# Kernel tuning notes

Measured on AMD Instinct MI355X. Metric: run time of the kernel, lower is better.

The kernel has to match this reference:

```python
import jax, jax.numpy as jnp
import numpy as np

LEAKY_SLOPE = 0.01  # torch.nn.LeakyReLU default negative_slope

N_NODES = 100000
LATENT = 64
N_EDGES = 3200000
HIDDEN = 32


def setup_inputs() -> dict:
    key = jax.random.key(0)
    k_z, k_e0, k_e1, k_w1, k_b1, k_w2, k_b2 = jax.random.split(key, 7)
    z = jax.random.normal(k_z, (N_NODES, LATENT), dtype=jnp.float32)
    edge_idx = jnp.stack([
        jax.random.randint(k_e0, (N_EDGES,), 0, N_NODES),
        jax.random.randint(k_e1, (N_EDGES,), 0, N_NODES),
    ]).astype(jnp.int64 if jax.config.jax_enable_x64 else jnp.int32)
    in_dim = 2 * LATENT
    # torch Linear default init: U(-1/sqrt(fan_in), 1/sqrt(fan_in))
    s1 = 1.0 / np.sqrt(in_dim)
    s2 = 1.0 / np.sqrt(HIDDEN)
    W1 = jax.random.uniform(k_w1, (in_dim, HIDDEN), minval=-s1, maxval=s1, dtype=jnp.float32)
    b1 = jax.random.uniform(k_b1, (HIDDEN,), minval=-s1, maxval=s1, dtype=jnp.float32)
    W2 = jax.random.uniform(k_w2, (HIDDEN, 1), minval=-s2, maxval=s2, dtype=jnp.float32)
    b2 = jax.random.uniform(k_b2, (1,), minval=-s2, maxval=s2, dtype=jnp.float32)
    return {"z": z, "edge_idx": edge_idx, "W1": W1, "b1": b1, "W2": W2, "b2": b2}


def reference(z, edge_idx, W1, b1, W2, b2):
    # Gather node pairs and concat: [E, 2*latent_dim]
    node_pairs = jnp.concatenate([z[edge_idx[0]], z[edge_idx[1]]], axis=1)
    # Linear -> LeakyReLU (Dropout is identity at inference) -> Linear -> tanh
    h = node_pairs @ W1 + b1                    # [E, hidden]
    h = jnp.where(h >= 0, h, LEAKY_SLOPE * h)   # LeakyReLU
    out = h @ W2 + b2                           # [E, 1]
    return jnp.tanh(out)
```

## Files before the change

### kernel.cpp

```cpp
#include <hip/hip_runtime.h>
#include <hip/hip_fp16.h>
#include <math.h>

#define LEAKY 0.01f

__device__ inline float fast_tanh(float x) {
    float e2 = __expf(2.0f * x);
    return 1.0f - 2.0f * __builtin_amdgcn_rcpf(e2 + 1.0f);
}

__device__ inline float2 h2f(uint w) {
    __half2 h = *reinterpret_cast<__half2*>(&w);
    return __half22float2(h);
}

__global__ __launch_bounds__(256) void node_proj_g4(
    const float* __restrict__ z, const float* __restrict__ W1,
    const float* __restrict__ b1, __half* __restrict__ U, __half* __restrict__ V,
    int N)
{
    __shared__ float w1s[128 * 32];

    {
        const float4* src = reinterpret_cast<const float4*>(W1);
        float4* dst = reinterpret_cast<float4*>(w1s);
        int tid = threadIdx.x;
        #pragma unroll
        for (int i = 0; i < 4; ++i) dst[tid + 256 * i] = src[tid + 256 * i];
    }
    __syncthreads();

    int t = blockIdx.x * blockDim.x + threadIdx.x;
    int n = t >> 2;
    int g = t & 3;
    if (n >= N) return;

    const float4* zr = reinterpret_cast<const float4*>(z + (size_t)n * 64);

    float au[8], av[8];
    #pragma unroll
    for (int j = 0; j < 8; ++j) { au[j] = b1[g * 8 + j]; av[j] = 0.0f; }

    #pragma unroll 4
    for (int k4 = 0; k4 < 16; ++k4) {
        float4 a = zr[k4];
        #pragma unroll
        for (int c = 0; c < 4; ++c) {
            int k = 4 * k4 + c;
            float zk = (c == 0) ? a.x : (c == 1) ? a.y : (c == 2) ? a.z : a.w;
            const float4* wu = reinterpret_cast<const float4*>(&w1s[k * 32 + g * 8]);
            const float4* wv = reinterpret_cast<const float4*>(&w1s[(64 + k) * 32 + g * 8]);
            float4 wu0 = wu[0], wu1 = wu[1];
            float4 wv0 = wv[0], wv1 = wv[1];
            au[0] = fmaf(zk, wu0.x, au[0]);
            au[1] = fmaf(zk, wu0.y, au[1]);
            au[2] = fmaf(zk, wu0.z, au[2]);
            au[3] = fmaf(zk, wu0.w, au[3]);
            au[4] = fmaf(zk, wu1.x, au[4]);
            au[5] = fmaf(zk, wu1.y, au[5]);
            au[6] = fmaf(zk, wu1.z, au[6]);
            au[7] = fmaf(zk, wu1.w, au[7]);
            av[0] = fmaf(zk, wv0.x, av[0]);
            av[1] = fmaf(zk, wv0.y, av[1]);
            av[2] = fmaf(zk, wv0.z, av[2]);
            av[3] = fmaf(zk, wv0.w, av[3]);
            av[4] = fmaf(zk, wv1.x, av[4]);
            av[5] = fmaf(zk, wv1.y, av[5]);
            av[6] = fmaf(zk, wv1.z, av[6]);
            av[7] = fmaf(zk, wv1.w, av[7]);
        }
    }

    uint wu[4], wv[4];
    #pragma unroll
    for (int i = 0; i < 4; ++i) {
        __half2 hu = __floats2half2_rn(au[2 * i], au[2 * i + 1]);
        wu[i] = *reinterpret_cast<uint*>(&hu);
        __half2 hv = __floats2half2_rn(av[2 * i], av[2 * i + 1]);
        wv[i] = *reinterpret_cast<uint*>(&hv);
    }
    *reinterpret_cast<uint4*>(U + (size_t)n * 32 + g * 8) = make_uint4(wu[0], wu[1], wu[2], wu[3]);
    *reinterpret_cast<uint4*>(V + (size_t)n * 32 + g * 8) = make_uint4(wv[0], wv[1], wv[2], wv[3]);
}

__device__ inline float edge_dot(uint4 uq, uint4 vq, float4 w2a, float4 w2b) {
    float acc = 0.0f;
    float2 uu, vv; float h0, h1;
    uu = h2f(uq.x); vv = h2f(vq.x);
    h0 = uu.x + vv.x; h1 = uu.y + vv.y;
    h0 = (h0 >= 0.0f) ? h0 : LEAKY * h0;
    h1 = (h1 >= 0.0f) ? h1 : LEAKY * h1;
    acc = fmaf(h0, w2a.x, acc); acc = fmaf(h1, w2a.y, acc);
    uu = h2f(uq.y); vv = h2f(vq.y);
    h0 = uu.x + vv.x; h1 = uu.y + vv.y;
    h0 = (h0 >= 0.0f) ? h0 : LEAKY * h0;
    h1 = (h1 >= 0.0f) ? h1 : LEAKY * h1;
    acc = fmaf(h0, w2a.z, acc); acc = fmaf(h1, w2a.w, acc);
    uu = h2f(uq.z); vv = h2f(vq.z);
    h0 = uu.x + vv.x; h1 = uu.y + vv.y;
    h0 = (h0 >= 0.0f) ? h0 : LEAKY * h0;
    h1 = (h1 >= 0.0f) ? h1 : LEAKY * h1;
    acc = fmaf(h0, w2b.x, acc); acc = fmaf(h1, w2b.y, acc);
    uu = h2f(uq.w); vv = h2f(vq.w);
    h0 = uu.x + vv.x; h1 = uu.y + vv.y;
    h0 = (h0 >= 0.0f) ? h0 : LEAKY * h0;
    h1 = (h1 >= 0.0f) ? h1 : LEAKY * h1;
    acc = fmaf(h0, w2b.z, acc); acc = fmaf(h1, w2b.w, acc);
    return acc;
}

__global__ __launch_bounds__(256) void edge_decode_q4(
    const int* __restrict__ idx,
    const __half* __restrict__ U, const __half* __restrict__ V,
    const float* __restrict__ W2, const float* __restrict__ b2,
    float* __restrict__ out, int E)
{
    int t = blockIdx.x * blockDim.x + threadIdx.x;
    int p = t & 3;
    int e0 = t & ~3;
    if (e0 >= E) return;
    int eN = E - 1;
    int ea = min(e0, eN), eb = min(e0 + 1, eN), ec = min(e0 + 2, eN), ed = min(e0 + 3, eN);

    int s0 = idx[ea], s1 = idx[eb], s2 = idx[ec], s3 = idx[ed];
    int d0 = idx[E + ea], d1 = idx[E + eb], d2 = idx[E + ec], d3 = idx[E + ed];

    const uint4* Up = reinterpret_cast<const uint4*>(U);
    const uint4* Vp = reinterpret_cast<const uint4*>(V);
    uint4 u0 = Up[(size_t)s0 * 4 + p];
    uint4 u1 = Up[(size_t)s1 * 4 + p];
    uint4 u2 = Up[(size_t)s2 * 4 + p];
    uint4 u3 = Up[(size_t)s3 * 4 + p];
    uint4 v0 = Vp[(size_t)d0 * 4 + p];
    uint4 v1 = Vp[(size_t)d1 * 4 + p];
    uint4 v2 = Vp[(size_t)d2 * 4 + p];
    uint4 v3 = Vp[(size_t)d3 * 4 + p];

    float4 w2a = *reinterpret_cast<const float4*>(W2 + p * 8);
    float4 w2b = *reinterpret_cast<const float4*>(W2 + p * 8 + 4);

    float a0 = edge_dot(u0, v0, w2a, w2b);
    float a1 = edge_dot(u1, v1, w2a, w2b);
    float a2 = edge_dot(u2, v2, w2a, w2b);
    float a3 = edge_dot(u3, v3, w2a, w2b);

    a0 += __shfl_xor(a0, 1); a0 += __shfl_xor(a0, 2);
    a1 += __shfl_xor(a1, 1); a1 += __shfl_xor(a1, 2);
    a2 += __shfl_xor(a2, 1); a2 += __shfl_xor(a2, 2);
    a3 += __shfl_xor(a3, 1); a3 += __shfl_xor(a3, 2);

    float r = (p == 0) ? a0 : (p == 1) ? a1 : (p == 2) ? a2 : a3;
    r = fast_tanh(r + b2[0]);
    int eo = e0 + p;
    if (eo < E) out[eo] = r;
}

__global__ __launch_bounds__(256) void edge_mlp_f32(
    const float* __restrict__ z, const int* __restrict__ idx,
    const float* __restrict__ W1, const float* __restrict__ b1,
    const float* __restrict__ W2, const float* __restrict__ b2,
    float* __restrict__ out, int E)
{
    int e = blockIdx.x * blockDim.x + threadIdx.x;
    if (e >= E) return;
    int s = idx[e];
    int d = idx[E + e];
    const float4* zs = reinterpret_cast<const float4*>(z + (size_t)s * 64);
    const float4* zd = reinterpret_cast<const float4*>(z + (size_t)d * 64);

    float h[32];
    #pragma unroll
    for (int j = 0; j < 32; ++j) h[j] = b1[j];

    #pragma unroll 4
    for (int k4 = 0; k4 < 16; ++k4) {
        float4 a = zs[k4];
        float4 b = zd[k4];
        const float* wa0 = W1 + (4 * k4 + 0) * 32;
        const float* wa1 = W1 + (4 * k4 + 1) * 32;
        const float* wa2 = W1 + (4 * k4 + 2) * 32;
        const float* wa3 = W1 + (4 * k4 + 3) * 32;
        const float* wb0 = W1 + (64 + 4 * k4 + 0) * 32;
        const float* wb1 = W1 + (64 + 4 * k4 + 1) * 32;
        const float* wb2 = W1 + (64 + 4 * k4 + 2) * 32;
        const float* wb3 = W1 + (64 + 4 * k4 + 3) * 32;
        #pragma unroll
        for (int j = 0; j < 32; ++j) {
            float acc = h[j];
            acc = fmaf(a.x, wa0[j], acc);
            acc = fmaf(a.y, wa1[j], acc);
            acc = fmaf(a.z, wa2[j], acc);
            acc = fmaf(a.w, wa3[j], acc);
            acc = fmaf(b.x, wb0[j], acc);
            acc = fmaf(b.y, wb1[j], acc);
            acc = fmaf(b.z, wb2[j], acc);
            acc = fmaf(b.w, wb3[j], acc);
            h[j] = acc;
        }
    }

    float acc = b2[0];
    #pragma unroll
    for (int j = 0; j < 32; ++j) {
        float hv = h[j];
        hv = (hv >= 0.0f) ? hv : LEAKY * hv;
        acc = fmaf(hv, W2[j], acc);
    }
    out[e] = tanhf(acc);
}

extern "C" void kernel_launch(void* const* d_in, const int* in_sizes, int n_in,
                              void* d_out, int out_size, void* d_ws, size_t ws_size,
                              hipStream_t stream) {
    const float* z  = (const float*)d_in[0];
    const int*   idx = (const int*)d_in[1];
    const float* W1 = (const float*)d_in[2];
    const float* b1 = (const float*)d_in[3];
    const float* W2 = (const float*)d_in[4];
    const float* b2 = (const float*)d_in[5];
    float* out = (float*)d_out;

    const int E = out_size;
    const int N = in_sizes[0] / 64;

    size_t need = (size_t)2 * N * 32 * sizeof(__half);
    if (ws_size >= need) {
        __half* U = (__half*)d_ws;
        __half* V = U + (size_t)N * 32;
        const int threads = 256;
        int nthread_np = 4 * N;
        node_proj_g4<<<(nthread_np + threads - 1) / threads, threads, 0, stream>>>(
            z, W1, b1, U, V, N);
        edge_decode_q4<<<(E + threads - 1) / threads, threads, 0, stream>>>(
            idx, U, V, W2, b2, out, E);
    } else {
        const int threads = 256;
        edge_mlp_f32<<<(E + threads - 1) / threads, threads, 0, stream>>>(
            z, idx, W1, b1, W2, b2, out, E);
    }
}
```

Measured before the change: 183.8 us.

## Compute node projection with bf16 MFMA instead of scalar FMA

Rewrites the per-node projection kernel to convert z rows and W1 to bf16 and compute the 64->64 projection (U and V halves) with 16x16x32 bf16 MFMA instructions, staging results through LDS for coalesced fp16 stores. This replaces the scalar fp32 FMA loop with matrix-core work. It adds bf16 rounding of inputs and weights, which can cost accuracy. The edge decode kernel, likely the dominant cost, is unchanged, so the overall effect depends on how much time the projection kernel takes.

Result: faster. 176.1 us (-4.2%).

```diff
diff --git a/kernel.cpp b/kernel.cpp
--- a/kernel.cpp
+++ b/kernel.cpp
@@ -1,8 +1,12 @@
 #include <hip/hip_runtime.h>
 #include <hip/hip_fp16.h>
+#include <hip/hip_bf16.h>
 #include <math.h>
 
 #define LEAKY 0.01f
+
+typedef __attribute__((ext_vector_type(8))) short short8v;
+typedef __attribute__((ext_vector_type(4))) float f32x4;
 
 __device__ inline float fast_tanh(float x) {
     float e2 = __expf(2.0f * x);
@@ -14,73 +18,111 @@
     return __half22float2(h);
 }
 
-__global__ __launch_bounds__(256) void node_proj_g4(
+__device__ inline short f2bf(float f) {
+    __hip_bfloat16 h = __float2bfloat16(f);
+    short s;
+    __builtin_memcpy(&s, &h, 2);
+    return s;
+}
+
+__global__ __launch_bounds__(256) void node_proj_mfma(
     const float* __restrict__ z, const float* __restrict__ W1,
     const float* __restrict__ b1, __half* __restrict__ U, __half* __restrict__ V,
     int N)
 {
-    __shared__ float w1s[128 * 32];
-
-    {
-        const float4* src = reinterpret_cast<const float4*>(W1);
-        float4* dst = reinterpret_cast<float4*>(w1s);
-        int tid = threadIdx.x;
-        #pragma unroll
-        for (int i = 0; i < 4; ++i) dst[tid + 256 * i] = src[tid + 256 * i];
+    __shared__ short w1l[64 * 72];
+    __shared__ __half st[4][64 * 88];
+
+    int tid = threadIdx.x;
+    int w = tid >> 6;
+    int l = tid & 63;
+
+    for (int i = tid; i < 4096; i += 256) {
+        int j = i >> 6;
+        int k = i & 63;
+        float wv = (j < 32) ? W1[k * 32 + j] : W1[(64 + k) * 32 + (j - 32)];
+        w1l[j * 72 + k] = f2bf(wv);
     }
     __syncthreads();
 
-    int t = blockIdx.x * blockDim.x + threadIdx.x;
-    int n = t >> 2;
-    int g = t & 3;
-    if (n >= N) return;
-
-    const float4* zr = reinterpret_cast<const float4*>(z + (size_t)n * 64);
-
-    float au[8], av[8];
-    #pragma unroll
-    for (int j = 0; j < 8; ++j) { au[j] = b1[g * 8 + j]; av[j] = 0.0f; }
-
-    #pragma unroll 4
-    for (int k4 = 0; k4 < 16; ++k4) {
-        float4 a = zr[k4];
-        #pragma unroll
-        for (int c = 0; c < 4; ++c) {
-            int k = 4 * k4 + c;
-            float zk = (c == 0) ? a.x : (c == 1) ? a.y : (c == 2) ? a.z : a.w;
-            const float4* wu = reinterpret_cast<const float4*>(&w1s[k * 32 + g * 8]);
-            const float4* wv = reinterpret_cast<const float4*>(&w1s[(64 + k) * 32 + g * 8]);
-            float4 wu0 = wu[0], wu1 = wu[1];
-            float4 wv0 = wv[0], wv1 = wv[1];
-            au[0] = fmaf(zk, wu0.x, au[0]);
-            au[1] = fmaf(zk, wu0.y, au[1]);
-            au[2] = fmaf(zk, wu0.z, au[2]);
-            au[3] = fmaf(zk, wu0.w, au[3]);
-            au[4] = fmaf(zk, wu1.x, au[4]);
-            au[5] = fmaf(zk, wu1.y, au[5]);
-            au[6] = fmaf(zk, wu1.z, au[6]);
-            au[7] = fmaf(zk, wu1.w, au[7]);
-            av[0] = fmaf(zk, wv0.x, av[0]);
-            av[1] = fmaf(zk, wv0.y, av[1]);
-            av[2] = fmaf(zk, wv0.z, av[2]);
-            av[3] = fmaf(zk, wv0.w, av[3]);
-            av[4] = fmaf(zk, wv1.x, av[4]);
-            av[5] = fmaf(zk, wv1.y, av[5]);
-            av[6] = fmaf(zk, wv1.z, av[6]);
-            av[7] = fmaf(zk, wv1.w, av[7]);
-        }
-    }
-
-    uint wu[4], wv[4];
-    #pragma unroll
-    for (int i = 0; i < 4; ++i) {
-        __half2 hu = __floats2half2_rn(au[2 * i], au[2 * i + 1]);
-        wu[i] = *reinterpret_cast<uint*>(&hu);
-        __half2 hv = __floats2half2_rn(av[2 * i], av[2 * i + 1]);
-        wv[i] = *reinterpret_cast<uint*>(&hv);
-    }
-    *reinterpret_cast<uint4*>(U + (size_t)n * 32 + g * 8) = make_uint4(wu[0], wu[1], wu[2], wu[3]);
-    *reinterpret_cast<uint4*>(V + (size_t)n * 32 + g * 8) = make_uint4(wv[0], wv[1], wv[2], wv[3]);
+    const float4* z4 = reinterpret_cast<const float4*>(z);
+    int rbase = blockIdx.x * 256 + w * 64 + (l & 15);
+    int koff = (l >> 4) * 8;
+    short8v afr[4][2];
+    #pragma unroll
+    for (int mi = 0; mi < 4; ++mi) {
+        int rg = rbase + mi * 16;
+        bool ok = rg < N;
+        size_t rowoff = (size_t)(ok ? rg : 0) * 16;
+        #pragma unroll
+        for (int kk = 0; kk < 2; ++kk) {
+            int kq = (kk * 32 + koff) >> 2;
+            float4 p0 = z4[rowoff + kq];
+            float4 p1 = z4[rowoff + kq + 1];
+            if (!ok) { p0 = make_float4(0, 0, 0, 0); p1 = make_float4(0, 0, 0, 0); }
+            short8v f;
+            f[0] = f2bf(p0.x); f[1] = f2bf(p0.y); f[2] = f2bf(p0.z); f[3] = f2bf(p0.w);
+            f[4] = f2bf(p1.x); f[5] = f2bf(p1.y); f[6] = f2bf(p1.z); f[7] = f2bf(p1.w);
+            afr[mi][kk] = f;
+        }
+    }
+
+    f32x4 acc[4][4];
+    #pragma unroll
+    for (int mi = 0; mi < 4; ++mi)
+        #pragma unroll
+        for (int ni = 0; ni < 4; ++ni)
+            acc[mi][ni] = (f32x4){0.0f, 0.0f, 0.0f, 0.0f};
+
+    #pragma unroll
+    for (int kk = 0; kk < 2; ++kk) {
+        short8v bfr[4];
+        #pragma unroll
+        for (int ni = 0; ni < 4; ++ni) {
+            int col = ni * 16 + (l & 15);
+            bfr[ni] = *reinterpret_cast<const short8v*>(&w1l[col * 72 + kk * 32 + koff]);
+        }
+        #pragma unroll
+        for (int mi = 0; mi < 4; ++mi)
+            #pragma unroll
+            for (int ni = 0; ni < 4; ++ni)
+                acc[mi][ni] = __builtin_amdgcn_mfma_f32_16x16x32_bf16(
+                    afr[mi][kk], bfr[ni], acc[mi][ni], 0, 0, 0);
+    }
+
+    float bc[4];
+    #pragma unroll
+    for (int ni = 0; ni < 4; ++ni) {
+        int col = ni * 16 + (l & 15);
+        bc[ni] = (col < 32) ? b1[col] : 0.0f;
+    }
+    __half* stw = &st[w][0];
+    #pragma unroll
+    for (int mi = 0; mi < 4; ++mi)
+        #pragma unroll
+        for (int ni = 0; ni < 4; ++ni)
+            #pragma unroll
+            for (int r = 0; r < 4; ++r) {
+                int row = mi * 16 + (l >> 4) * 4 + r;
+                int col = ni * 16 + (l & 15);
+                stw[row * 88 + col] = __float2half(acc[mi][ni][r] + bc[ni]);
+            }
+    __syncthreads();
+
+    int nb = blockIdx.x * 256 + w * 64;
+    #pragma unroll
+    for (int i = 0; i < 8; ++i) {
+        int rl = i * 8 + (l >> 3);
+        int c = l & 7;
+        int n = nb + rl;
+        if (n < N) {
+            uint4 val = *reinterpret_cast<const uint4*>(&stw[rl * 88 + c * 8]);
+            if (c < 4)
+                *reinterpret_cast<uint4*>(U + (size_t)n * 32 + c * 8) = val;
+            else
+                *reinterpret_cast<uint4*>(V + (size_t)n * 32 + (c - 4) * 8) = val;
+        }
+    }
 }
 
 __device__ inline float edge_dot(uint4 uq, uint4 vq, float4 w2a, float4 w2b) {
@@ -228,9 +270,8 @@
         __half* U = (__half*)d_ws;
         __half* V = U + (size_t)N * 32;
         const int threads = 256;
-        int nthread_np = 4 * N;
-        node_proj_g4<<<(nthread_np + threads - 1) / threads, threads, 0, stream>>>(
-            z, W1, b1, U, V, N);
+        int nblocks_np = (N + 255) / 256;
+        node_proj_mfma<<<nblocks_np, threads, 0, stream>>>(z, W1, b1, U, V, N);
         edge_decode_q4<<<(E + threads - 1) / threads, threads, 0, stream>>>(
             idx, U, V, W2, b2, out, E);
     } else {
```
